# Kernel optimization log

Measured on AMD Instinct MI355X. Metric: run time of the kernel, lower is better.

The kernel has to match this reference:

```python
import jax, jax.numpy as jnp
import numpy as np

N = 50000
E = 800000
D_IN = 128
D_HID = 128
D_OUT = 64
BN_EPS = 1e-5


def setup_inputs() -> dict:
    key = jax.random.key(0)
    ks = jax.random.split(key, 16)
    s = lambda k, shp, fan: jax.random.normal(k, shp, dtype=jnp.float32) / np.sqrt(fan)
    return {
        "x": jax.random.normal(ks[0], (N, D_IN), dtype=jnp.float32),
        "edge_index": jax.random.randint(ks[1], (2, E), 0, N, dtype=jnp.int64),
        # layer 1: SAGEConv(in -> hid)
        "w1l": s(ks[2], (D_IN, D_HID), D_IN),
        "w1r": s(ks[3], (D_IN, D_HID), D_IN),
        "b1": jnp.zeros((D_HID,), jnp.float32),
        "g1": jnp.ones((D_HID,), jnp.float32),
        "be1": jnp.zeros((D_HID,), jnp.float32),
        # layer 2: SAGEConv(hid -> hid)
        "w2l": s(ks[4], (D_HID, D_HID), D_HID),
        "w2r": s(ks[5], (D_HID, D_HID), D_HID),
        "b2": jnp.zeros((D_HID,), jnp.float32),
        "g2": jnp.ones((D_HID,), jnp.float32),
        "be2": jnp.zeros((D_HID,), jnp.float32),
        # layer 3: SAGEConv(hid -> out)
        "w3l": s(ks[6], (D_HID, D_OUT), D_HID),
        "w3r": s(ks[7], (D_HID, D_OUT), D_HID),
        "b3": jnp.zeros((D_OUT,), jnp.float32),
    }


def sage_conv(x, src, dst, wl, wr, b):
    # mean aggregation of source-node features onto destination nodes
    msg_sum = jax.ops.segment_sum(x[src], dst, num_segments=N)  # [N, d]
    deg = jax.ops.segment_sum(jnp.ones((src.shape[0],), x.dtype), dst, num_segments=N)
    mean = msg_sum / jnp.maximum(deg, 1.0)[:, None]
    return mean @ wl + x @ wr + b


def batch_norm(x, g, b):
    mu = jnp.mean(x, axis=0)
    var = jnp.var(x, axis=0)
    return (x - mu) * jax.lax.rsqrt(var + BN_EPS) * g + b


def reference(x, edge_index, w1l, w1r, b1, g1, be1, w2l, w2r, b2, g2, be2, w3l, w3r, b3):
    src, dst = edge_index[0], edge_index[1]
    h = sage_conv(x, src, dst, w1l, w1r, b1)
    h = jax.nn.relu(batch_norm(h, g1, be1))
    h = sage_conv(h, src, dst, w2l, w2r, b2)
    h = jax.nn.relu(batch_norm(h, g2, be2))
    return sage_conv(h, src, dst, w3l, w3r, b3)
```

## Files before the change

### kernel.cpp

```cpp
#include <hip/hip_runtime.h>
#include <hip/hip_bf16.h>

#define NN 50000
#define NE 800000
#define DH 128
#define NB1 196
#define NBK 391
#define EPB 4096
#define CAPB 4096

typedef __attribute__((ext_vector_type(8))) short bf16x8;
typedef __attribute__((ext_vector_type(4))) float f32x4;
typedef __attribute__((ext_vector_type(8))) unsigned short us8;
typedef __attribute__((ext_vector_type(4))) unsigned short us4;

__device__ __forceinline__ unsigned short f2bf(float f) {
  unsigned int u = __builtin_bit_cast(unsigned int, f);
  unsigned int r = (u + 0x7FFFu + ((u >> 16) & 1u)) >> 16;
  return (unsigned short)r;
}
__device__ __forceinline__ float bf2f(unsigned int h16) {
  unsigned int u = h16 << 16;
  return __builtin_bit_cast(float, u);
}

__global__ __launch_bounds__(256) void k_prep(const float* __restrict__ x,
                                              const float* __restrict__ w1l, const float* __restrict__ w1r,
                                              const float* __restrict__ w2l, const float* __restrict__ w2r,
                                              const float* __restrict__ w3l, const float* __restrict__ w3r,
                                              unsigned short* __restrict__ xb,
                                              unsigned short* __restrict__ w1t,
                                              unsigned short* __restrict__ w2t,
                                              unsigned short* __restrict__ w3t) {
  int b = blockIdx.x, t = threadIdx.x;
  if (b < 3125) {
    int i = b * 256 + t;
    const float4* p = reinterpret_cast<const float4*>(x) + (size_t)i * 2;
    float4 a = p[0], bb = p[1];
    us8 o;
    o[0] = f2bf(a.x); o[1] = f2bf(a.y); o[2] = f2bf(a.z); o[3] = f2bf(a.w);
    o[4] = f2bf(bb.x); o[5] = f2bf(bb.y); o[6] = f2bf(bb.z); o[7] = f2bf(bb.w);
    reinterpret_cast<us8*>(xb)[i] = o;
  } else if (b < 3381) {
    bool is1 = b < 3253;
    int idx = (b - (is1 ? 3125 : 3253)) * 256 + t;
    int c = idx >> 8, k = idx & 255;
    const float* wl = is1 ? w1l : w2l;
    const float* wr = is1 ? w1r : w2r;
    float v = (k < DH) ? wl[k * DH + c] : wr[(k - DH) * DH + c];
    (is1 ? w1t : w2t)[idx] = f2bf(v);
  } else {
    int idx = (b - 3381) * 256 + t;
    int c = idx >> 7, k = idx & 127;
    float v = (c < 64) ? w3l[k * 64 + c] : w3r[k * 64 + (c - 64)];
    w3t[idx] = f2bf(v);
  }
}

__global__ __launch_bounds__(256) void k_bucket(const int* __restrict__ src,
                                                const int* __restrict__ dst,
                                                int* __restrict__ deg,
                                                int* __restrict__ bcnt,
                                                int* __restrict__ ebuf) {
  __shared__ int lcnt[NBK], lbase[NBK];
  int t = threadIdx.x;
  for (int b = t; b < NBK; b += 256) lcnt[b] = 0;
  __syncthreads();
  int base = blockIdx.x * EPB;
  int d[16], s[16];
#pragma unroll
  for (int i = 0; i < 16; ++i) {
    int e = base + i * 256 + t;
    if (e < NE) { d[i] = dst[e]; s[i] = src[e]; }
    else d[i] = -1;
  }
#pragma unroll
  for (int i = 0; i < 16; ++i)
    if (d[i] >= 0) {
      atomicAdd(&deg[d[i]], 1);
      atomicAdd(&lcnt[d[i] >> 7], 1);
    }
  __syncthreads();
  for (int b = t; b < NBK; b += 256) {
    int c = lcnt[b];
    lbase[b] = c > 0 ? atomicAdd(&bcnt[b], c) : 0;
    lcnt[b] = 0;
  }
  __syncthreads();
#pragma unroll
  for (int i = 0; i < 16; ++i) {
    if (d[i] >= 0) {
      int b = d[i] >> 7;
      int r = atomicAdd(&lcnt[b], 1);
      ebuf[(size_t)b * CAPB + lbase[b] + r] = s[i] | ((d[i] & 127) << 20);
    }
  }
}

__global__ void k_scan1(const int* __restrict__ deg, int* __restrict__ iscan,
                        int* __restrict__ bsum) {
  __shared__ int s[256];
  int t = threadIdx.x;
  int i = blockIdx.x * 256 + t;
  int d = (i < NN) ? deg[i] : 0;
  s[t] = d;
  __syncthreads();
  for (int off = 1; off < 256; off <<= 1) {
    int v = (t >= off) ? s[t - off] : 0;
    __syncthreads();
    s[t] += v;
    __syncthreads();
  }
  if (i < NN) iscan[i] = s[t];
  if (t == 255) bsum[blockIdx.x] = s[255];
}

__global__ void k_scan2(int* __restrict__ bsum) {
  __shared__ int s[256];
  int t = threadIdx.x;
  int v = (t < NB1) ? bsum[t] : 0;
  s[t] = v;
  __syncthreads();
  for (int off = 1; off < 256; off <<= 1) {
    int u = (t >= off) ? s[t - off] : 0;
    __syncthreads();
    s[t] += u;
    __syncthreads();
  }
  if (t < NB1) bsum[t] = s[t] - v;
}

__global__ void k_scan3(const int* __restrict__ deg, const int* __restrict__ iscan,
                        const int* __restrict__ bsum, int* __restrict__ rowptr,
                        float* __restrict__ invd) {
  int i = blockIdx.x * 256 + threadIdx.x;
  if (i >= NN) return;
  int d = deg[i];
  int excl = bsum[blockIdx.x] + iscan[i] - d;
  rowptr[i] = excl;
  invd[i] = 1.0f / (float)(d > 0 ? d : 1);
  if (i == 0) rowptr[NN] = NE;
}

__global__ __launch_bounds__(256) void k_fill2(const int* __restrict__ rowptr,
                                               const int* __restrict__ bcnt,
                                               const int* __restrict__ ebuf,
                                               int* __restrict__ adj) {
  int b = blockIdx.x;
  int n0 = b << 7;
  int n1 = n0 + 128; if (n1 > NN) n1 = NN;
  __shared__ int cur[128];
  int t = threadIdx.x;
  if (t < n1 - n0) cur[t] = rowptr[n0 + t];
  __syncthreads();
  int cnt = bcnt[b];
  const int* eb = ebuf + (size_t)b * CAPB;
  for (int e = t; e < cnt; e += 256) {
    int p = eb[e];
    int pos = atomicAdd(&cur[(p >> 20) & 127], 1);
    adj[pos] = p & 0xFFFFF;
  }
}

template <bool BNA>
__global__ __launch_bounds__(256) void k_agg(const unsigned short* __restrict__ h,
                                             const int* __restrict__ rowptr,
                                             const int* __restrict__ adj,
                                             const float* __restrict__ invd,
                                             const float* __restrict__ stats,
                                             const float* __restrict__ g,
                                             const float* __restrict__ be,
                                             unsigned short* __restrict__ meanb) {
  int wid = (blockIdx.x * blockDim.x + threadIdx.x) >> 6;
  int lane = threadIdx.x & 63;
  if (wid >= NN) return;
  int lo = rowptr[wid], hi = rowptr[wid + 1];
  int q = lane >> 4;
  int c = (lane & 15) << 3;
  float sc[8], sh[8];
  if (BNA) {
#pragma unroll
    for (int j = 0; j < 8; ++j) {
      int col = c + j;
      float mu = stats[col] * (1.0f / NN);
      float var = stats[128 + col] * (1.0f / NN) - mu * mu;
      float rs = rsqrtf(var + 1e-5f);
      sc[j] = rs * g[col];
      sh[j] = be[col] - mu * sc[j];
    }
  }
  float a[8] = {};
  int e = lo;
#pragma unroll 2
  for (; e + 4 <= hi; e += 4) {
    int s = adj[e + q];
    us8 v = *reinterpret_cast<const us8*>(h + (size_t)s * DH + c);
#pragma unroll
    for (int j = 0; j < 8; ++j) {
      float f = bf2f(v[j]);
      a[j] += BNA ? fmaxf(f * sc[j] + sh[j], 0.0f) : f;
    }
  }
  if (q < hi - e) {
    int s = adj[e + q];
    us8 v = *reinterpret_cast<const us8*>(h + (size_t)s * DH + c);
#pragma unroll
    for (int j = 0; j < 8; ++j) {
      float f = bf2f(v[j]);
      a[j] += BNA ? fmaxf(f * sc[j] + sh[j], 0.0f) : f;
    }
  }
#pragma unroll
  for (int j = 0; j < 8; ++j) {
    a[j] += __shfl_xor(a[j], 16);
    a[j] += __shfl_xor(a[j], 32);
  }
  if (q == 0) {
    float iv = invd[wid];
    us8 o;
#pragma unroll
    for (int j = 0; j < 8; ++j) o[j] = f2bf(a[j] * iv);
    *reinterpret_cast<us8*>(meanb + (size_t)wid * DH + c) = o;
  }
}

__global__ __launch_bounds__(256) void k_agg3(const unsigned short* __restrict__ t3,
                                              const int* __restrict__ rowptr,
                                              const int* __restrict__ adj,
                                              const float* __restrict__ invd,
                                              const float* __restrict__ b3,
                                              float* __restrict__ out) {
  int wid = (blockIdx.x * blockDim.x + threadIdx.x) >> 6;
  int lane = threadIdx.x & 63;
  if (wid >= NN) return;
  int lo = rowptr[wid], hi = rowptr[wid + 1];
  int q = lane >> 4;
  int c = (lane & 15) << 2;
  float a[4] = {};
  int e = lo;
#pragma unroll 2
  for (; e + 4 <= hi; e += 4) {
    int s = adj[e + q];
    us4 v = *reinterpret_cast<const us4*>(t3 + (size_t)s * 128 + c);
#pragma unroll
    for (int j = 0; j < 4; ++j) a[j] += bf2f(v[j]);
  }
  if (q < hi - e) {
    int s = adj[e + q];
    us4 v = *reinterpret_cast<const us4*>(t3 + (size_t)s * 128 + c);
#pragma unroll
    for (int j = 0; j < 4; ++j) a[j] += bf2f(v[j]);
  }
#pragma unroll
  for (int j = 0; j < 4; ++j) {
    a[j] += __shfl_xor(a[j], 16);
    a[j] += __shfl_xor(a[j], 32);
  }
  if (q == 0) {
    float iv = invd[wid];
    us4 w = *reinterpret_cast<const us4*>(t3 + (size_t)wid * 128 + 64 + c);
    float4 o;
    o.x = a[0] * iv + bf2f(w[0]) + b3[c + 0];
    o.y = a[1] * iv + bf2f(w[1]) + b3[c + 1];
    o.z = a[2] * iv + bf2f(w[2]) + b3[c + 2];
    o.w = a[3] * iv + bf2f(w[3]) + b3[c + 3];
    *reinterpret_cast<float4*>(out + (size_t)wid * 64 + c) = o;
  }
}

template <bool SPLIT, bool STATS, bool APPLY>
__global__ __launch_bounds__(256) void k_gemm(const unsigned short* __restrict__ Am,
                                              const unsigned short* __restrict__ Ah,
                                              const unsigned short* __restrict__ Wt,
                                              const float* __restrict__ bias,
                                              const float* __restrict__ stA,
                                              const float* __restrict__ gA,
                                              const float* __restrict__ beA,
                                              unsigned short* __restrict__ outb,
                                              float* __restrict__ stats) {
  constexpr int KS = SPLIT ? 8 : 4;
  constexpr int WK = KS * 32;
  __shared__ float asc[DH], ash[DH];
  if (APPLY) {
    int t = threadIdx.x;
    if (t < DH) {
      float mu = stA[t] * (1.0f / NN);
      float var = stA[128 + t] * (1.0f / NN) - mu * mu;
      float rs = rsqrtf(var + 1e-5f);
      float scv = rs * gA[t];
      asc[t] = scv;
      ash[t] = beA[t] - mu * scv;
    }
    __syncthreads();
  }
  int lane = threadIdx.x & 63;
  int w = threadIdx.x >> 6;
  int wr = w >> 1, wc = w & 1;
  int rowbase = blockIdx.x * 128 + wr * 64;
  int colbase = wc * 64;
  int lr = lane & 15, lk = (lane >> 4) << 3;

  f32x4 acc[4][4] = {};
#pragma unroll
  for (int ks = 0; ks < KS; ++ks) {
    const unsigned short* Ab = (!SPLIT || ks < 4) ? Am : Ah;
    bool tr = APPLY && (!SPLIT || ks >= 4);
    int ka = ((ks & 3) << 5) + lk;
    int kw = (ks << 5) + lk;
    bf16x8 af[4], bfr[4];
#pragma unroll
    for (int i = 0; i < 4; ++i) {
      int r = rowbase + i * 16 + lr;
      r = r < NN ? r : NN - 1;
      us8 raw = *reinterpret_cast<const us8*>(Ab + (size_t)r * DH + ka);
      if (tr) {
        us8 o;
#pragma unroll
        for (int j = 0; j < 8; ++j) {
          float f = bf2f(raw[j]);
          o[j] = f2bf(fmaxf(f * asc[ka + j] + ash[ka + j], 0.0f));
        }
        af[i] = __builtin_bit_cast(bf16x8, o);
      } else {
        af[i] = __builtin_bit_cast(bf16x8, raw);
      }
    }
#pragma unroll
    for (int j = 0; j < 4; ++j)
      bfr[j] = *reinterpret_cast<const bf16x8*>(Wt + (size_t)(colbase + j * 16 + lr) * WK + kw);
#pragma unroll
    for (int i = 0; i < 4; ++i)
#pragma unroll
      for (int j = 0; j < 4; ++j)
        acc[i][j] = __builtin_amdgcn_mfma_f32_16x16x32_bf16(af[i], bfr[j], acc[i][j], 0, 0, 0);
  }

  float bv[4];
#pragma unroll
  for (int j = 0; j < 4; ++j) bv[j] = bias ? bias[colbase + j * 16 + lr] : 0.0f;

  float s1[4] = {}, s2[4] = {};
#pragma unroll
  for (int i = 0; i < 4; ++i) {
#pragma unroll
    for (int j = 0; j < 4; ++j) {
      int col = colbase + j * 16 + lr;
#pragma unroll
      for (int r = 0; r < 4; ++r) {
        int row = rowbase + i * 16 + ((lane >> 4) << 2) + r;
        if (row < NN) {
          float val = acc[i][j][r] + bv[j];
          outb[(size_t)row * 128 + col] = f2bf(val);
          if (STATS) { s1[j] += val; s2[j] += val * val; }
        }
      }
    }
  }

  if (STATS) {
    __shared__ float sd[2][128][2];
#pragma unroll
    for (int j = 0; j < 4; ++j) {
      s1[j] += __shfl_xor(s1[j], 16);
      s1[j] += __shfl_xor(s1[j], 32);
      s2[j] += __shfl_xor(s2[j], 16);
      s2[j] += __shfl_xor(s2[j], 32);
    }
    if (lane < 16) {
#pragma unroll
      for (int j = 0; j < 4; ++j) {
        sd[wr][colbase + j * 16 + lane][0] = s1[j];
        sd[wr][colbase + j * 16 + lane][1] = s2[j];
      }
    }
    __syncthreads();
    int t = threadIdx.x;
    if (t < 128) {
      atomicAdd(&stats[t], sd[0][t][0] + sd[1][t][0]);
      atomicAdd(&stats[128 + t], sd[0][t][1] + sd[1][t][1]);
    }
  }
}

extern "C" void kernel_launch(void* const* d_in, const int* in_sizes, int n_in,
                              void* d_out, int out_size, void* d_ws, size_t ws_size,
                              hipStream_t stream) {
  const float* x = (const float*)d_in[0];
  const int* ei = (const int*)d_in[1];
  const int* srcp = ei;
  const int* dstp = ei + NE;
  const float* w1l = (const float*)d_in[2];
  const float* w1r = (const float*)d_in[3];
  const float* b1 = (const float*)d_in[4];
  const float* g1 = (const float*)d_in[5];
  const float* be1 = (const float*)d_in[6];
  const float* w2l = (const float*)d_in[7];
  const float* w2r = (const float*)d_in[8];
  const float* b2 = (const float*)d_in[9];
  const float* g2 = (const float*)d_in[10];
  const float* be2 = (const float*)d_in[11];
  const float* w3l = (const float*)d_in[12];
  const float* w3r = (const float*)d_in[13];
  const float* b3 = (const float*)d_in[14];

  char* ws = (char*)d_ws;
  size_t off = 0;
  auto alloc = [&](size_t bytes) {
    char* p = ws + off;
    off = (off + bytes + 255) & ~(size_t)255;
    return p;
  };
  unsigned short* xb = (unsigned short*)alloc((size_t)NN * DH * 2);
  unsigned short* meanb = (unsigned short*)alloc((size_t)NN * DH * 2);
  unsigned short* gbuf1 = (unsigned short*)alloc((size_t)NN * DH * 2);
  unsigned short* gbuf2 = (unsigned short*)alloc((size_t)NN * DH * 2);
  unsigned short* w1t = (unsigned short*)alloc(128 * 256 * 2);
  unsigned short* w2t = (unsigned short*)alloc(128 * 256 * 2);
  unsigned short* w3t = (unsigned short*)alloc(128 * 128 * 2);
  int* deg = (int*)alloc(NN * 4);
  int* bcnt = (int*)alloc(NBK * 4);
  float* stats1 = (float*)alloc(2 * DH * 4);
  float* stats2 = (float*)alloc(2 * DH * 4);
  size_t zlen = (char*)(stats2 + 2 * DH) - (char*)deg;
  int* rowptr = (int*)alloc((NN + 1) * 4);
  int* adj = (int*)alloc((size_t)NE * 4);
  int* ebuf = (int*)alloc((size_t)NBK * CAPB * 4);
  float* invd = (float*)alloc(NN * 4);
  int* iscan = (int*)alloc(NN * 4);
  int* bsum = (int*)alloc(NB1 * 4);

  hipMemsetAsync(deg, 0, zlen, stream);
  k_prep<<<3445, 256, 0, stream>>>(x, w1l, w1r, w2l, w2r, w3l, w3r, xb, w1t, w2t, w3t);
  k_bucket<<<(NE + EPB - 1) / EPB, 256, 0, stream>>>(srcp, dstp, deg, bcnt, ebuf);
  k_scan1<<<NB1, 256, 0, stream>>>(deg, iscan, bsum);
  k_scan2<<<1, 256, 0, stream>>>(bsum);
  k_scan3<<<NB1, 256, 0, stream>>>(deg, iscan, bsum, rowptr, invd);
  k_fill2<<<NBK, 256, 0, stream>>>(rowptr, bcnt, ebuf, adj);

  int agg_blocks = (NN * 64 + 255) / 256;
  int gemm_blocks = (NN + 127) / 128;

  k_agg<false><<<agg_blocks, 256, 0, stream>>>(xb, rowptr, adj, invd, nullptr, nullptr, nullptr, meanb);
  k_gemm<true, true, false><<<gemm_blocks, 256, 0, stream>>>(
      meanb, xb, w1t, b1, nullptr, nullptr, nullptr, gbuf1, stats1);

  k_agg<true><<<agg_blocks, 256, 0, stream>>>(gbuf1, rowptr, adj, invd, stats1, g1, be1, meanb);
  k_gemm<true, true, true><<<gemm_blocks, 256, 0, stream>>>(
      meanb, gbuf1, w2t, b2, stats1, g1, be1, gbuf2, stats2);

  k_gemm<false, false, true><<<gemm_blocks, 256, 0, stream>>>(
      gbuf2, nullptr, w3t, nullptr, stats2, g2, be2, gbuf1, nullptr);
  k_agg3<<<agg_blocks, 256, 0, stream>>>(gbuf1, rowptr, adj, invd, b3, (float*)d_out);
}
```

Baseline: 245.8 us.

## Replace global degree atomics with per-bucket shared-memory histogram kernel

Removes the 800K global atomicAdds on the degree array from the bucketing kernel and instead computes per-node degrees in a new kernel that histograms each bucket's edge buffer in shared memory, also writing inverse degrees there. Edges per bucketing block are halved to raise block count and parallelism. This trades contended global atomics for an extra kernel launch and an extra pass over the bucketed edge buffer.

```diff
diff --git a/kernel.cpp b/kernel.cpp
--- a/kernel.cpp
+++ b/kernel.cpp
@@ -6,7 +6,7 @@
 #define DH 128
 #define NB1 196
 #define NBK 391
-#define EPB 4096
+#define EPB 2048
 #define CAPB 4096
 
 typedef __attribute__((ext_vector_type(8))) short bf16x8;
@@ -59,7 +59,6 @@
 
 __global__ __launch_bounds__(256) void k_bucket(const int* __restrict__ src,
                                                 const int* __restrict__ dst,
-                                                int* __restrict__ deg,
                                                 int* __restrict__ bcnt,
                                                 int* __restrict__ ebuf) {
   __shared__ int lcnt[NBK], lbase[NBK];
@@ -67,19 +66,16 @@
   for (int b = t; b < NBK; b += 256) lcnt[b] = 0;
   __syncthreads();
   int base = blockIdx.x * EPB;
-  int d[16], s[16];
-#pragma unroll
-  for (int i = 0; i < 16; ++i) {
+  int d[8], s[8];
+#pragma unroll
+  for (int i = 0; i < 8; ++i) {
     int e = base + i * 256 + t;
     if (e < NE) { d[i] = dst[e]; s[i] = src[e]; }
     else d[i] = -1;
   }
 #pragma unroll
-  for (int i = 0; i < 16; ++i)
-    if (d[i] >= 0) {
-      atomicAdd(&deg[d[i]], 1);
-      atomicAdd(&lcnt[d[i] >> 7], 1);
-    }
+  for (int i = 0; i < 8; ++i)
+    if (d[i] >= 0) atomicAdd(&lcnt[d[i] >> 7], 1);
   __syncthreads();
   for (int b = t; b < NBK; b += 256) {
     int c = lcnt[b];
@@ -88,12 +84,34 @@
   }
   __syncthreads();
 #pragma unroll
-  for (int i = 0; i < 16; ++i) {
+  for (int i = 0; i < 8; ++i) {
     if (d[i] >= 0) {
       int b = d[i] >> 7;
       int r = atomicAdd(&lcnt[b], 1);
       ebuf[(size_t)b * CAPB + lbase[b] + r] = s[i] | ((d[i] & 127) << 20);
     }
+  }
+}
+
+__global__ __launch_bounds__(256) void k_hist(const int* __restrict__ bcnt,
+                                              const int* __restrict__ ebuf,
+                                              int* __restrict__ deg,
+                                              float* __restrict__ invd) {
+  int b = blockIdx.x;
+  __shared__ int h[128];
+  int t = threadIdx.x;
+  if (t < 128) h[t] = 0;
+  __syncthreads();
+  int cnt = bcnt[b];
+  const int* eb = ebuf + (size_t)b * CAPB;
+  for (int e = t; e < cnt; e += 256)
+    atomicAdd(&h[(eb[e] >> 20) & 127], 1);
+  __syncthreads();
+  int i = (b << 7) + t;
+  if (t < 128 && i < NN) {
+    int d = h[t];
+    deg[i] = d;
+    invd[i] = 1.0f / (float)(d > 0 ? d : 1);
   }
 }
 
@@ -131,14 +149,11 @@
 }
 
 __global__ void k_scan3(const int* __restrict__ deg, const int* __restrict__ iscan,
-                        const int* __restrict__ bsum, int* __restrict__ rowptr,
-                        float* __restrict__ invd) {
+                        const int* __restrict__ bsum, int* __restrict__ rowptr) {
   int i = blockIdx.x * 256 + threadIdx.x;
   if (i >= NN) return;
-  int d = deg[i];
-  int excl = bsum[blockIdx.x] + iscan[i] - d;
+  int excl = bsum[blockIdx.x] + iscan[i] - deg[i];
   rowptr[i] = excl;
-  invd[i] = 1.0f / (float)(d > 0 ? d : 1);
   if (i == 0) rowptr[NN] = NE;
 }
 
@@ -417,11 +432,11 @@
   unsigned short* w1t = (unsigned short*)alloc(128 * 256 * 2);
   unsigned short* w2t = (unsigned short*)alloc(128 * 256 * 2);
   unsigned short* w3t = (unsigned short*)alloc(128 * 128 * 2);
-  int* deg = (int*)alloc(NN * 4);
   int* bcnt = (int*)alloc(NBK * 4);
   float* stats1 = (float*)alloc(2 * DH * 4);
   float* stats2 = (float*)alloc(2 * DH * 4);
-  size_t zlen = (char*)(stats2 + 2 * DH) - (char*)deg;
+  size_t zlen = (char*)(stats2 + 2 * DH) - (char*)bcnt;
+  int* deg = (int*)alloc(NN * 4);
   int* rowptr = (int*)alloc((NN + 1) * 4);
   int* adj = (int*)alloc((size_t)NE * 4);
   int* ebuf = (int*)alloc((size_t)NBK * CAPB * 4);
@@ -429,12 +444,13 @@
   int* iscan = (int*)alloc(NN * 4);
   int* bsum = (int*)alloc(NB1 * 4);
 
-  hipMemsetAsync(deg, 0, zlen, stream);
+  hipMemsetAsync(bcnt, 0, zlen, stream);
   k_prep<<<3445, 256, 0, stream>>>(x, w1l, w1r, w2l, w2r, w3l, w3r, xb, w1t, w2t, w3t);
-  k_bucket<<<(NE + EPB - 1) / EPB, 256, 0, stream>>>(srcp, dstp, deg, bcnt, ebuf);
+  k_bucket<<<(NE + EPB - 1) / EPB, 256, 0, stream>>>(srcp, dstp, bcnt, ebuf);
+  k_hist<<<NBK, 256, 0, stream>>>(bcnt, ebuf, deg, invd);
   k_scan1<<<NB1, 256, 0, stream>>>(deg, iscan, bsum);
   k_scan2<<<1, 256, 0, stream>>>(bsum);
-  k_scan3<<<NB1, 256, 0, stream>>>(deg, iscan, bsum, rowptr, invd);
+  k_scan3<<<NB1, 256, 0, stream>>>(deg, iscan, bsum, rowptr);
   k_fill2<<<NBK, 256, 0, stream>>>(rowptr, bcnt, ebuf, adj);
 
   int agg_blocks = (NN * 64 + 255) / 256;
```

After: 221.8 us. 1.11x faster.
